# Optimization experiments

Measured on AMD Instinct MI355X. Metric: run time of the kernel, lower is better.

## Reference

```python
import jax, jax.numpy as jnp
import numpy as np

B, C, H, W = 32, 3072, 28, 28   # concatenated layer4(upsampled)+layer3 features of ResNet-50 @448px
K = 11                          # num_cpt concepts (prototypes)
NC = 200                        # num_classes (CUB-200)


def setup_inputs() -> dict:
    key = jax.random.key(0)
    k0, k1, k2 = jax.random.split(key, 3)
    x = jax.random.normal(k0, (B, C, H, W), dtype=jnp.float32)
    # fc_landmarks: 1x1 conv, no bias -> weight (K, C)
    w_land = jax.random.normal(k1, (K, C), dtype=jnp.float32) * 0.02
    # modulation parameter, initialized to ones in the module
    modulation = jnp.ones((1, C, K), dtype=jnp.float32)
    # fc_class_landmarks: Linear(C -> NC), no bias -> weight (NC, C)
    w_cls = jax.random.normal(k2, (NC, C), dtype=jnp.float32) * 0.02
    return {"x": x, "w_land": w_land, "modulation": modulation, "w_cls": w_cls}


def reference(x, w_land, modulation, w_cls):
    # ab = fc_landmarks(x): 1x1 conv == channel contraction
    ab = jnp.einsum('bchw,kc->bkhw', x, w_land)                      # (B,K,H,W)
    b_sq = jnp.sum(x * x, axis=1, keepdims=True)                     # (B,1,H,W)
    a_sq = jnp.sum(w_land * w_land, axis=1)[None, :, None, None]     # (1,K,1,1)
    # squared distance ||x - w||^2 = b_sq - 2ab + a_sq; softmax over concepts of -dist
    maps = jax.nn.softmax(-(b_sq - 2.0 * ab + a_sq), axis=1)         # (B,K,H,W)
    attn_cls = jnp.sum(maps, axis=(-2, -1))                          # (B,K)
    # (maps.unsqueeze(1) * x.unsqueeze(2)).mean(-1).mean(-1) == batched contraction over HW
    hw = maps.shape[-2] * maps.shape[-1]
    all_features = jnp.einsum('bkhw,bchw->bck', maps, x) / hw        # (B,C,K)
    all_features_modulated = all_features * modulation               # (B,C,K)
    # eval mode: Dropout1d is identity
    scores = jnp.einsum('bck,nc->bnk', all_features_modulated, w_cls)  # (B,NC,K)
    scores = jnp.sum(scores, axis=-1)                                # (B,NC)
    return all_features_modulated, scores, maps, attn_cls
```

## Files before the change

kernel.cpp:

```cpp
#include <hip/hip_runtime.h>

constexpr int B  = 32;
constexpr int C  = 3072;
constexpr int HW = 784;
constexpr int K  = 11;
constexpr int NC = 200;

constexpr int AFM_OFF    = 0;
constexpr int SCORES_OFF = 1081344;
constexpr int MAPS_OFF   = 1087744;
constexpr int ATTN_OFF   = 1363712;

constexpr int WT_OFF   = 0;
constexpr int ASQ_OFF  = 36864;
constexpr int FSUM_OFF = 36880;

__global__ __launch_bounds__(256) void k0_prep(const float* __restrict__ w_land,
                                               float* __restrict__ ws) {
  const int bid = blockIdx.x;
  const int t = threadIdx.x;
  if (bid < K) {
    const int k = bid;
    float s = 0.f;
    for (int c = t; c < C; c += 256) {
      float v = w_land[k * C + c];
      s = fmaf(v, v, s);
    }
    __shared__ float red[256];
    red[t] = s;
    __syncthreads();
    for (int off = 128; off > 0; off >>= 1) {
      if (t < off) red[t] += red[t + off];
      __syncthreads();
    }
    if (t == 0) ws[ASQ_OFF + k] = red[0];
  } else {
    const int c = (bid - K) * 256 + t;
    #pragma unroll
    for (int k = 0; k < K; k++)
      ws[WT_OFF + c * 12 + k] = 2.f * w_land[k * C + c];
    ws[WT_OFF + c * 12 + K] = 0.f;
  }
}

__global__ __launch_bounds__(512) void k1_maps(const float* __restrict__ x,
                                               const float* __restrict__ ws,
                                               float* __restrict__ maps_out,
                                               float* __restrict__ attn_out) {
  const int bid  = blockIdx.x;
  const int b    = bid / 13;
  const int tile = bid % 13;
  const int t    = threadIdx.x;
  const int g    = __builtin_amdgcn_readfirstlane(t >> 6);
  const int hwl  = t & 63;
  const int hw   = tile * 64 + hwl;
  const int hwc  = hw < HW ? hw : HW - 1;

  const float* xp  = x + (size_t)b * C * HW + hwc;
  const float* wT  = ws + WT_OFF;
  const float* asq = ws + ASQ_OFF;

  float acc[K];
  #pragma unroll
  for (int k = 0; k < K; k++) acc[k] = (g == 0) ? -asq[k] : 0.f;

  for (int i0 = 0; i0 < C / 8; i0 += 8) {
    float xv[8];
    #pragma unroll
    for (int u = 0; u < 8; u++)
      xv[u] = xp[(size_t)((i0 + u) * 8 + g) * HW];
    #pragma unroll
    for (int u = 0; u < 8; u++) {
      const float* wrow = wT + ((i0 + u) * 8 + g) * 12;
      #pragma unroll
      for (int k = 0; k < K; k++) acc[k] = fmaf(wrow[k], xv[u], acc[k]);
    }
  }

  __shared__ float abp[8][K][64];
  #pragma unroll
  for (int k = 0; k < K; k++) abp[g][k][hwl] = acc[k];
  __syncthreads();

  if (g == 0) {
    float l[K];
    #pragma unroll
    for (int k = 0; k < K; k++) {
      float s = 0.f;
      #pragma unroll
      for (int gg = 0; gg < 8; gg++) s += abp[gg][k][hwl];
      l[k] = s;
    }
    float m = l[0];
    #pragma unroll
    for (int k = 1; k < K; k++) m = fmaxf(m, l[k]);
    float z = 0.f;
    #pragma unroll
    for (int k = 0; k < K; k++) { l[k] = __expf(l[k] - m); z += l[k]; }
    const float inv = 1.f / z;
    const bool valid = hw < HW;
    #pragma unroll
    for (int k = 0; k < K; k++) {
      float r = l[k] * inv;
      if (valid) maps_out[((size_t)b * K + k) * HW + hw] = r;
      float v = valid ? r : 0.f;
      #pragma unroll
      for (int sh = 32; sh > 0; sh >>= 1) v += __shfl_xor(v, sh);
      if (hwl == 0) atomicAdd(&attn_out[b * K + k], v);
    }
  }
}

constexpr int CT   = 128;
constexpr int XROW = 68;
constexpr int MROW = 832;

__global__ __launch_bounds__(256) void k2_feat(const float* __restrict__ x,
                                               const float* __restrict__ maps_g,
                                               const float* __restrict__ modulation,
                                               float* __restrict__ afm_out) {
  __shared__ __align__(16) float maps_s[K * MROW];
  __shared__ __align__(16) float lds_x[CT * XROW];

  const int bid = blockIdx.x;
  const int b   = (B - 1) - (bid / (C / CT));
  const int c0  = (bid % (C / CT)) * CT;
  const int t   = threadIdx.x;

  for (int k = 0; k < K; k++)
    for (int i = t; i < MROW; i += 256)
      maps_s[k * MROW + i] = (i < HW) ? maps_g[((size_t)b * K + k) * HW + i] : 0.f;

  const int hwl = t & 63;
  const int rr  = t >> 6;
  const int p   = t & 63;
  const int q   = t >> 6;

  float f0[K], f1[K];
  #pragma unroll
  for (int k = 0; k < K; k++) { f0[k] = 0.f; f1[k] = 0.f; }

  const float* xb = x + (size_t)b * C * HW;

  for (int ch = 0; ch < 13; ch++) {
    const int hbase = ch * 64;
    __syncthreads();
    #pragma unroll
    for (int i = 0; i < CT / 4; i++) {
      const int r = rr + i * 4;
      int hwp = hbase + hwl;
      if (hwp >= HW) hwp = HW - 1;
      lds_x[r * XROW + hwl] = xb[(size_t)(c0 + r) * HW + hwp];
    }
    __syncthreads();
    #pragma unroll
    for (int hg = 0; hg < 4; hg++) {
      const int hoff = (q * 4 + hg) * 4;
      const float4 xa = *(const float4*)&lds_x[p * XROW + hoff];
      const float4 xc = *(const float4*)&lds_x[(p + 64) * XROW + hoff];
      #pragma unroll
      for (int k = 0; k < K; k++) {
        const float4 m4 = *(const float4*)&maps_s[k * MROW + hbase + hoff];
        f0[k] += xa.x * m4.x + xa.y * m4.y + xa.z * m4.z + xa.w * m4.w;
        f1[k] += xc.x * m4.x + xc.y * m4.y + xc.z * m4.z + xc.w * m4.w;
      }
    }
  }

  __syncthreads();
  float* fbuf = lds_x;
  #pragma unroll
  for (int k = 0; k < K; k++) {
    fbuf[(q * CT + p) * K + k]      = f0[k];
    fbuf[(q * CT + p + 64) * K + k] = f1[k];
  }
  __syncthreads();

  const float inv_hw = 1.f / (float)HW;
  for (int o = t; o < CT * K; o += 256) {
    float s = fbuf[o] + fbuf[CT * K + o] + fbuf[2 * CT * K + o] + fbuf[3 * CT * K + o];
    afm_out[(size_t)b * C * K + c0 * K + o] = s * inv_hw * modulation[c0 * K + o];
  }
}

__global__ __launch_bounds__(256) void k3_fsum(const float* __restrict__ afm,
                                               float* __restrict__ fsum) {
  const int i = blockIdx.x * 256 + threadIdx.x;
  const float* p = afm + (size_t)i * K;
  float s = 0.f;
  #pragma unroll
  for (int k = 0; k < K; k++) s += p[k];
  fsum[i] = s;
}

__global__ __launch_bounds__(256) void k4_scores(const float* __restrict__ fsum,
                                                 const float* __restrict__ w_cls,
                                                 float* __restrict__ scores) {
  __shared__ float fs[C];
  const int bid = blockIdx.x;
  const int b   = bid / (NC / 8);
  const int nt  = bid % (NC / 8);
  const int t   = threadIdx.x;

  for (int i = t; i < C; i += 256) fs[i] = fsum[b * C + i];
  __syncthreads();

  const int nl = t >> 5, lane = t & 31;
  const int n = nt * 8 + nl;
  const float* wr = w_cls + (size_t)n * C;
  float acc = 0.f;
  for (int c = lane; c < C; c += 32) acc = fmaf(wr[c], fs[c], acc);
  #pragma unroll
  for (int sh = 16; sh > 0; sh >>= 1) acc += __shfl_xor(acc, sh);
  if (lane == 0) scores[b * NC + n] = acc;
}

extern "C" void kernel_launch(void* const* d_in, const int* in_sizes, int n_in,
                              void* d_out, int out_size, void* d_ws, size_t ws_size,
                              hipStream_t stream) {
  const float* x          = (const float*)d_in[0];
  const float* w_land     = (const float*)d_in[1];
  const float* modulation = (const float*)d_in[2];
  const float* w_cls      = (const float*)d_in[3];

  float* out    = (float*)d_out;
  float* afm    = out + AFM_OFF;
  float* scores = out + SCORES_OFF;
  float* maps   = out + MAPS_OFF;
  float* attn   = out + ATTN_OFF;
  float* ws     = (float*)d_ws;

  hipMemsetAsync(attn, 0, B * K * sizeof(float), stream);
  k0_prep  <<<K + C / 256,     256, 0, stream>>>(w_land, ws);
  k1_maps  <<<B * 13,          512, 0, stream>>>(x, ws, maps, attn);
  k2_feat  <<<B * (C / CT),    256, 0, stream>>>(x, maps, modulation, afm);
  k3_fsum  <<<(B * C) / 256,   256, 0, stream>>>(afm, ws + FSUM_OFF);
  k4_scores<<<B * (NC / 8),    256, 0, stream>>>(ws + FSUM_OFF, w_cls, scores);
}
```

Baseline: 565.7 us.

## Retile maps kernel, prefetch x in feature kernel, fuse fsum into it

The maps kernel now splits HW into 16 tiles (one of 64 and fifteen of 48) so 512 blocks cover the GPU more evenly, and each wave group reads a contiguous channel range instead of strided channels. The feature kernel loads x with float4 global reads into registers for the next HW chunk while computing the current one, acting as a software prefetch, and it loads maps as float4. The per-channel feature sum is folded into the feature kernel's epilogue, which removes the separate fsum launch and its re-read of afm. The cost is more registers held for prefetch and some idle lanes in the 48-wide tiles.

```diff
diff --git a/kernel.cpp b/kernel.cpp
--- a/kernel.cpp
+++ b/kernel.cpp
@@ -48,15 +48,17 @@
                                                float* __restrict__ maps_out,
                                                float* __restrict__ attn_out) {
   const int bid  = blockIdx.x;
-  const int b    = bid / 13;
-  const int tile = bid % 13;
+  const int b    = bid >> 4;
+  const int tile = bid & 15;
   const int t    = threadIdx.x;
   const int g    = __builtin_amdgcn_readfirstlane(t >> 6);
   const int hwl  = t & 63;
-  const int hw   = tile * 64 + hwl;
-  const int hwc  = hw < HW ? hw : HW - 1;
-
-  const float* xp  = x + (size_t)b * C * HW + hwc;
+  const int hw0  = (tile == 0) ? 0 : 16 + tile * 48;
+  const int tsz  = (tile == 0) ? 64 : 48;
+  const bool valid = hwl < tsz;
+  const int hw   = hw0 + (valid ? hwl : (tsz - 1));
+
+  const float* xp  = x + (size_t)b * C * HW + hw;
   const float* wT  = ws + WT_OFF;
   const float* asq = ws + ASQ_OFF;
 
@@ -64,14 +66,15 @@
   #pragma unroll
   for (int k = 0; k < K; k++) acc[k] = (g == 0) ? -asq[k] : 0.f;
 
+  const int cbase = g * (C / 8);
   for (int i0 = 0; i0 < C / 8; i0 += 8) {
     float xv[8];
     #pragma unroll
     for (int u = 0; u < 8; u++)
-      xv[u] = xp[(size_t)((i0 + u) * 8 + g) * HW];
+      xv[u] = xp[(size_t)(cbase + i0 + u) * HW];
     #pragma unroll
     for (int u = 0; u < 8; u++) {
-      const float* wrow = wT + ((i0 + u) * 8 + g) * 12;
+      const float* wrow = wT + (cbase + i0 + u) * 12;
       #pragma unroll
       for (int k = 0; k < K; k++) acc[k] = fmaf(wrow[k], xv[u], acc[k]);
     }
@@ -98,7 +101,6 @@
     #pragma unroll
     for (int k = 0; k < K; k++) { l[k] = __expf(l[k] - m); z += l[k]; }
     const float inv = 1.f / z;
-    const bool valid = hw < HW;
     #pragma unroll
     for (int k = 0; k < K; k++) {
       float r = l[k] * inv;
@@ -118,7 +120,8 @@
 __global__ __launch_bounds__(256) void k2_feat(const float* __restrict__ x,
                                                const float* __restrict__ maps_g,
                                                const float* __restrict__ modulation,
-                                               float* __restrict__ afm_out) {
+                                               float* __restrict__ afm_out,
+                                               float* __restrict__ fsum_out) {
   __shared__ __align__(16) float maps_s[K * MROW];
   __shared__ __align__(16) float lds_x[CT * XROW];
 
@@ -127,32 +130,51 @@
   const int c0  = (bid % (C / CT)) * CT;
   const int t   = threadIdx.x;
 
-  for (int k = 0; k < K; k++)
-    for (int i = t; i < MROW; i += 256)
-      maps_s[k * MROW + i] = (i < HW) ? maps_g[((size_t)b * K + k) * HW + i] : 0.f;
-
-  const int hwl = t & 63;
-  const int rr  = t >> 6;
-  const int p   = t & 63;
-  const int q   = t >> 6;
+  if (t < MROW / 4) {
+    float4 v = make_float4(0.f, 0.f, 0.f, 0.f);
+    #pragma unroll
+    for (int k = 0; k < K; k++) {
+      if (t < HW / 4)
+        v = ((const float4*)(maps_g + ((size_t)b * K + k) * HW))[t];
+      else
+        v = make_float4(0.f, 0.f, 0.f, 0.f);
+      ((float4*)(maps_s + k * MROW))[t] = v;
+    }
+  }
+
+  const int f4l  = t & 15;
+  const int rgrp = t >> 4;
+  const int p    = t & 63;
+  const int q    = t >> 6;
+
+  const float4* xb4 = (const float4*)(x + (size_t)b * C * HW);
+
+  float4 pf[8];
+  auto stage_load = [&](int ch) {
+    const int hb4 = ch * 16;
+    int c4 = hb4 + f4l;
+    if (c4 >= HW / 4) c4 = HW / 4 - 1;
+    #pragma unroll
+    for (int j = 0; j < 8; j++)
+      pf[j] = xb4[(size_t)(c0 + rgrp + j * 16) * (HW / 4) + c4];
+  };
+  auto stage_write = [&]() {
+    #pragma unroll
+    for (int j = 0; j < 8; j++)
+      *(float4*)&lds_x[(rgrp + j * 16) * XROW + f4l * 4] = pf[j];
+  };
 
   float f0[K], f1[K];
   #pragma unroll
   for (int k = 0; k < K; k++) { f0[k] = 0.f; f1[k] = 0.f; }
 
-  const float* xb = x + (size_t)b * C * HW;
+  stage_load(0);
+  stage_write();
+  __syncthreads();
 
   for (int ch = 0; ch < 13; ch++) {
+    if (ch < 12) stage_load(ch + 1);
     const int hbase = ch * 64;
-    __syncthreads();
-    #pragma unroll
-    for (int i = 0; i < CT / 4; i++) {
-      const int r = rr + i * 4;
-      int hwp = hbase + hwl;
-      if (hwp >= HW) hwp = HW - 1;
-      lds_x[r * XROW + hwl] = xb[(size_t)(c0 + r) * HW + hwp];
-    }
-    __syncthreads();
     #pragma unroll
     for (int hg = 0; hg < 4; hg++) {
       const int hoff = (q * 4 + hg) * 4;
@@ -165,9 +187,13 @@
         f1[k] += xc.x * m4.x + xc.y * m4.y + xc.z * m4.z + xc.w * m4.w;
       }
     }
-  }
-
-  __syncthreads();
+    __syncthreads();
+    if (ch < 12) {
+      stage_write();
+      __syncthreads();
+    }
+  }
+
   float* fbuf = lds_x;
   #pragma unroll
   for (int k = 0; k < K; k++) {
@@ -181,16 +207,16 @@
     float s = fbuf[o] + fbuf[CT * K + o] + fbuf[2 * CT * K + o] + fbuf[3 * CT * K + o];
     afm_out[(size_t)b * C * K + c0 * K + o] = s * inv_hw * modulation[c0 * K + o];
   }
-}
-
-__global__ __launch_bounds__(256) void k3_fsum(const float* __restrict__ afm,
-                                               float* __restrict__ fsum) {
-  const int i = blockIdx.x * 256 + threadIdx.x;
-  const float* p = afm + (size_t)i * K;
-  float s = 0.f;
-  #pragma unroll
-  for (int k = 0; k < K; k++) s += p[k];
-  fsum[i] = s;
+  for (int cl = t; cl < CT; cl += 256) {
+    float s = 0.f;
+    #pragma unroll
+    for (int k = 0; k < K; k++) {
+      const int o = cl * K + k;
+      float v = fbuf[o] + fbuf[CT * K + o] + fbuf[2 * CT * K + o] + fbuf[3 * CT * K + o];
+      s += v * modulation[c0 * K + o];
+    }
+    fsum_out[(size_t)b * C + c0 + cl] = s * inv_hw;
+  }
 }
 
 __global__ __launch_bounds__(256) void k4_scores(const float* __restrict__ fsum,
@@ -232,8 +258,7 @@
 
   hipMemsetAsync(attn, 0, B * K * sizeof(float), stream);
   k0_prep  <<<K + C / 256,     256, 0, stream>>>(w_land, ws);
-  k1_maps  <<<B * 13,          512, 0, stream>>>(x, ws, maps, attn);
-  k2_feat  <<<B * (C / CT),    256, 0, stream>>>(x, maps, modulation, afm);
-  k3_fsum  <<<(B * C) / 256,   256, 0, stream>>>(afm, ws + FSUM_OFF);
+  k1_maps  <<<B * 16,          512, 0, stream>>>(x, ws, maps, attn);
+  k2_feat  <<<B * (C / CT),    256, 0, stream>>>(x, maps, modulation, afm, ws + FSUM_OFF);
   k4_scores<<<B * (NC / 8),    256, 0, stream>>>(ws + FSUM_OFF, w_cls, scores);
 }
```

Measured after the change: 625.4 us. 10.6% more time.
